# Kernel tuning notes

Hardware: AMD Instinct MI355X
Metric: run time of the kernel (lower is better)

The kernel has to match this reference:

```python
import jax, jax.numpy as jnp
import numpy as np

EPS = 1e-4


def bin_act(x):
    # row-wise standardize (torch std is unbiased, ddof=1) then XNOR-style binarize
    mu = x.mean(axis=1, keepdims=True)
    sd = x.std(axis=1, ddof=1, keepdims=True)
    xn = (x - mu) / (sd + EPS)
    alpha = jnp.abs(xn).mean(axis=1, keepdims=True)  # L1 norm / n
    return alpha * jnp.sign(xn)


def bin_linear(inp, w, b):
    # BinLinearFunction.forward: w_hat = sign(w) * (||w_row||_1 / n_in)
    n = w.shape[1]
    m = jnp.abs(w).sum(axis=1, keepdims=True) / n
    w_hat = jnp.sign(w) * m
    return inp @ w_hat.T + b


def scatter_mean(feat, dst, n_dst):
    s = jax.ops.segment_sum(feat, dst, num_segments=n_dst)
    cnt = jax.ops.segment_sum(jnp.ones(dst.shape, feat.dtype), dst, num_segments=n_dst)
    return s / jnp.maximum(cnt, 1.0)[:, None]


def sage_layer(x, src, dst, n_dst, w_rel, b_rel, w_root, b_root):
    xb = bin_act(x)
    xt = bin_act(x[:n_dst])
    agg = scatter_mean(xb[src], dst, n_dst)  # mean aggregation of binarized neighbors
    return bin_linear(agg, w_rel, b_rel) + bin_linear(xt, w_root, b_root)


def setup_inputs() -> dict:
    key = jax.random.key(0)
    ks = jax.random.split(key, 10)
    N0, N1, N2 = 512000, 20480, 2048
    E1, E2 = 512000, 20480
    IN, HID, OUT = 128, 256, 64
    x = jax.random.normal(ks[0], (N0, IN), dtype=jnp.float32)
    src1 = jax.random.randint(ks[1], (E1,), 0, N0)
    dst1 = jax.random.randint(ks[2], (E1,), 0, N1)
    src2 = jax.random.randint(ks[3], (E2,), 0, N1)
    dst2 = jax.random.randint(ks[4], (E2,), 0, N2)
    def winit(k, out_f, in_f):
        return jax.random.normal(k, (out_f, in_f), dtype=jnp.float32) * np.sqrt(1.0 / in_f)
    return {
        "x": x, "src1": src1, "dst1": dst1, "src2": src2, "dst2": dst2,
        "w_rel1": winit(ks[5], HID, IN), "b_rel1": jnp.zeros((HID,), jnp.float32),
        "w_root1": winit(ks[6], HID, IN), "b_root1": jnp.zeros((HID,), jnp.float32),
        "w_rel2": winit(ks[7], OUT, HID), "b_rel2": jnp.zeros((OUT,), jnp.float32),
        "w_root2": winit(ks[8], OUT, HID), "b_root2": jnp.zeros((OUT,), jnp.float32),
        "n1": N1, "n2": N2,
    }


def reference(x, src1, dst1, src2, dst2, w_rel1, b_rel1, w_root1, b_root1,
              w_rel2, b_rel2, w_root2, b_root2, n1, n2):
    h = sage_layer(x, src1, dst1, n1, w_rel1, b_rel1, w_root1, b_root1)
    h = jax.nn.relu(h)  # dropout p=0.0
    h = sage_layer(h, src2, dst2, n2, w_rel2, b_rel2, w_root2, b_root2)
    return jax.nn.log_softmax(h, axis=-1)
```

## Files before the change

kernel.cpp:

```cpp
#include <hip/hip_runtime.h>
#include <stdint.h>

typedef unsigned long long u64;


#define CAP1 128
#define CAP2 128

__device__ __forceinline__ void pack_row128(
    float4 v0, float4 v1, float4 v2, float4 v3, float mu, int c,
    u64& w0, u64& w1)
{
  unsigned m = 0;
  m |= (v0.x > mu) ? 1u << 0  : 0u;
  m |= (v0.y > mu) ? 1u << 1  : 0u;
  m |= (v0.z > mu) ? 1u << 2  : 0u;
  m |= (v0.w > mu) ? 1u << 3  : 0u;
  m |= (v1.x > mu) ? 1u << 4  : 0u;
  m |= (v1.y > mu) ? 1u << 5  : 0u;
  m |= (v1.z > mu) ? 1u << 6  : 0u;
  m |= (v1.w > mu) ? 1u << 7  : 0u;
  m |= (v2.x > mu) ? 1u << 8  : 0u;
  m |= (v2.y > mu) ? 1u << 9  : 0u;
  m |= (v2.z > mu) ? 1u << 10 : 0u;
  m |= (v2.w > mu) ? 1u << 11 : 0u;
  m |= (v3.x > mu) ? 1u << 12 : 0u;
  m |= (v3.y > mu) ? 1u << 13 : 0u;
  m |= (v3.z > mu) ? 1u << 14 : 0u;
  m |= (v3.w > mu) ? 1u << 15 : 0u;
  u64 wv = (u64)m << (16 * (c & 3));
  wv |= __shfl_xor(wv, 1);
  wv |= __shfl_xor(wv, 2);
  u64 other = __shfl_xor(wv, 4);
  w0 = (c & 4) ? other : wv;
  w1 = (c & 4) ? wv : other;
}

__device__ __forceinline__ void prep_w128_block(
    const float* __restrict__ w, int rowbase, int tid,
    ulonglong2* __restrict__ wbits, float* __restrict__ m)
{
  int lane = tid & 63;
  int g = lane >> 3, c = lane & 7;
  int row = rowbase + (tid >> 6) * 8 + g;
  const float4* wr = (const float4*)(w + (size_t)row * 128);
  float4 v0 = wr[c];
  float4 v1 = wr[c + 8];
  float4 v2 = wr[c + 16];
  float4 v3 = wr[c + 24];
  float s = fabsf(v0.x) + fabsf(v0.y) + fabsf(v0.z) + fabsf(v0.w)
          + fabsf(v1.x) + fabsf(v1.y) + fabsf(v1.z) + fabsf(v1.w)
          + fabsf(v2.x) + fabsf(v2.y) + fabsf(v2.z) + fabsf(v2.w)
          + fabsf(v3.x) + fabsf(v3.y) + fabsf(v3.z) + fabsf(v3.w);
  s += __shfl_xor(s, 1); s += __shfl_xor(s, 2); s += __shfl_xor(s, 4);
  u64 w0, w1;
  pack_row128(v0, v1, v2, v3, 0.0f, c, w0, w1);
  if (c == 0) {
    wbits[row] = make_ulonglong2(w0, w1);
    m[row] = s * (1.0f / 128.0f);
  }
}

__device__ __forceinline__ void prep_w256_block(
    const float* __restrict__ w, int rowbase, int tid,
    u64* __restrict__ wbits, float* __restrict__ m)
{
  int lane = tid & 63;
  int o = rowbase + (tid >> 6);
  const float* wr = w + (size_t)o * 256;
  float s = 0.0f;
  u64 b[4];
  #pragma unroll
  for (int wd = 0; wd < 4; wd++) {
    float v = wr[wd * 64 + lane];
    s += fabsf(v);
    b[wd] = __ballot(v > 0.0f);
  }
  #pragma unroll
  for (int off = 32; off > 0; off >>= 1) s += __shfl_xor(s, off);
  if (lane == 0) {
    wbits[o * 4 + 0] = b[0]; wbits[o * 4 + 1] = b[1];
    wbits[o * 4 + 2] = b[2]; wbits[o * 4 + 3] = b[3];
    m[o] = s * (1.0f / 256.0f);
  }
}

__global__ __launch_bounds__(256) void prep_all_kernel(
    const float* __restrict__ w_rel1, const float* __restrict__ w_root1,
    const float* __restrict__ w_rel2, const float* __restrict__ w_root2,
    ulonglong2* __restrict__ wbr1, float* __restrict__ m_r1,
    ulonglong2* __restrict__ wbt1, float* __restrict__ m_t1,
    u64* __restrict__ wbr2, float* __restrict__ m_r2,
    u64* __restrict__ wbt2, float* __restrict__ m_t2,
    int* __restrict__ cnt, int cntn)
{
  int b = blockIdx.x, t = threadIdx.x;
  if (b < 8) {
    prep_w128_block(w_rel1, b * 32, t, wbr1, m_r1);
  } else if (b < 16) {
    prep_w128_block(w_root1, (b - 8) * 32, t, wbt1, m_t1);
  } else if (b < 32) {
    prep_w256_block(w_rel2, (b - 16) * 4, t, wbr2, m_r2);
  } else if (b < 48) {
    prep_w256_block(w_root2, (b - 32) * 4, t, wbt2, m_t2);
  } else {
    int base = (b - 48) * 2048 + t * 8;
    #pragma unroll
    for (int k = 0; k < 8; k++) {
      int i = base + k;
      if (i < cntn) cnt[i] = 0;
    }
  }
}

__global__ void scatter_direct_kernel(
    const int* __restrict__ dst1, const int* __restrict__ src1, int E1,
    int* __restrict__ cnt1, int* __restrict__ slots1,
    const int* __restrict__ dst2, const int* __restrict__ src2, int E2,
    int* __restrict__ cnt2, int* __restrict__ slots2)
{
  int i = blockIdx.x * blockDim.x + threadIdx.x;
  if (i < E1) {
    int dd = dst1[i];
    int p = atomicAdd(&cnt1[dd], 1);
    if (p < CAP1) slots1[(size_t)dd * CAP1 + p] = src1[i];
  } else if (i < E1 + E2) {
    int j = i - E1;
    int dd = dst2[j];
    int p = atomicAdd(&cnt2[dd], 1);
    if (p < CAP2) slots2[(size_t)dd * CAP2 + p] = src2[j];
  }
}

__global__ __launch_bounds__(256) void binact128_kernel(
    const float* __restrict__ x, ulonglong2* __restrict__ bits1,
    float* __restrict__ alpha1)
{
  int lane = threadIdx.x & 63;
  int wid  = blockIdx.x * 4 + (threadIdx.x >> 6);
  int g = lane >> 3;
  int c = lane & 7;
  int row = wid * 8 + g;
  const float4* xr = (const float4*)(x + (size_t)row * 128);
  float4 v0 = xr[c];
  float4 v1 = xr[c + 8];
  float4 v2 = xr[c + 16];
  float4 v3 = xr[c + 24];

  float s = (v0.x + v0.y + v0.z + v0.w) + (v1.x + v1.y + v1.z + v1.w)
          + (v2.x + v2.y + v2.z + v2.w) + (v3.x + v3.y + v3.z + v3.w);
  s += __shfl_xor(s, 1); s += __shfl_xor(s, 2); s += __shfl_xor(s, 4);
  float mu = s * (1.0f / 128.0f);

  float ss = 0.f, sa = 0.f;
  {
    float d;
    d = v0.x - mu; ss += d * d; sa += fabsf(d);
    d = v0.y - mu; ss += d * d; sa += fabsf(d);
    d = v0.z - mu; ss += d * d; sa += fabsf(d);
    d = v0.w - mu; ss += d * d; sa += fabsf(d);
    d = v1.x - mu; ss += d * d; sa += fabsf(d);
    d = v1.y - mu; ss += d * d; sa += fabsf(d);
    d = v1.z - mu; ss += d * d; sa += fabsf(d);
    d = v1.w - mu; ss += d * d; sa += fabsf(d);
    d = v2.x - mu; ss += d * d; sa += fabsf(d);
    d = v2.y - mu; ss += d * d; sa += fabsf(d);
    d = v2.z - mu; ss += d * d; sa += fabsf(d);
    d = v2.w - mu; ss += d * d; sa += fabsf(d);
    d = v3.x - mu; ss += d * d; sa += fabsf(d);
    d = v3.y - mu; ss += d * d; sa += fabsf(d);
    d = v3.z - mu; ss += d * d; sa += fabsf(d);
    d = v3.w - mu; ss += d * d; sa += fabsf(d);
  }
  ss += __shfl_xor(ss, 1); ss += __shfl_xor(ss, 2); ss += __shfl_xor(ss, 4);
  sa += __shfl_xor(sa, 1); sa += __shfl_xor(sa, 2); sa += __shfl_xor(sa, 4);
  float sd = sqrtf(ss * (1.0f / 127.0f));
  float a  = __fdividef(sa * (1.0f / 128.0f), sd + 1e-4f);

  u64 w0, w1;
  pack_row128(v0, v1, v2, v3, mu, c, w0, w1);
  if (c == 0) {
    bits1[row] = make_ulonglong2(w0, w1);
    alpha1[row] = a;
  }
}

__global__ __launch_bounds__(256) void layer1_kernel(
    const ulonglong2* __restrict__ bits1, const float* __restrict__ alpha1,
    const int* __restrict__ cnt, const int* __restrict__ slots,
    const ulonglong2* __restrict__ wb_rel, const float* __restrict__ m_rel,
    const float* __restrict__ b_rel,
    const ulonglong2* __restrict__ wb_root, const float* __restrict__ m_root,
    const float* __restrict__ b_root,
    u64* __restrict__ bits2, float* __restrict__ alpha2)
{
  int lane = threadIdx.x & 63;
  int d = blockIdx.x * 4 + (threadIdx.x >> 6);

  ulonglong2 wr[4], wt[4];
  float mr[4], br[4], mt[4], bt[4];
  #pragma unroll
  for (int j = 0; j < 4; j++) {
    int f = j * 64 + lane;
    wr[j] = wb_rel[f];  mr[j] = m_rel[f];  br[j] = b_rel[f];
    wt[j] = wb_root[f]; mt[j] = m_root[f]; bt[j] = b_root[f];
  }

  int deg = cnt[d];
  int degc = min(deg, CAP1);
  const int* slot = slots + (size_t)d * CAP1;

  float acc2[4] = {0.f, 0.f, 0.f, 0.f};
  float suma = 0.f;

  #pragma unroll 4
  for (int e = 0; e < degc; e++) {
    int sn = __builtin_amdgcn_readfirstlane(slot[e]);
    ulonglong2 bb = bits1[sn];
    float a = alpha1[sn];
    suma += a;
    #pragma unroll
    for (int j = 0; j < 4; j++) {
      int pc = __popcll(bb.x ^ wr[j].x) + __popcll(bb.y ^ wr[j].y);
      acc2[j] += a * (float)pc;
    }
  }

  ulonglong2 xb = bits1[d];
  float ax = alpha1[d];

  float invc = (deg > 0) ? 1.0f / (float)deg : 1.0f;
  float z[4];
  #pragma unroll
  for (int j = 0; j < 4; j++) {
    int pcr = __popcll(xb.x ^ wt[j].x) + __popcll(xb.y ^ wt[j].y);
    float rel = mr[j] * (128.0f * suma - 2.0f * acc2[j]) * invc + br[j];
    float rot = mt[j] * ax * (float)(128 - 2 * pcr) + bt[j];
    z[j] = fmaxf(rel + rot, 0.0f);
  }

  float s = z[0] + z[1] + z[2] + z[3];
  #pragma unroll
  for (int off = 1; off < 64; off <<= 1) s += __shfl_xor(s, off);
  float mu = s * (1.0f / 256.0f);
  float ss = 0.f, sa = 0.f;
  #pragma unroll
  for (int j = 0; j < 4; j++) {
    float dv = z[j] - mu;
    ss += dv * dv; sa += fabsf(dv);
  }
  #pragma unroll
  for (int off = 1; off < 64; off <<= 1) {
    ss += __shfl_xor(ss, off);
    sa += __shfl_xor(sa, off);
  }
  float sd = sqrtf(ss * (1.0f / 255.0f));
  float a2 = __fdividef(sa * (1.0f / 256.0f), sd + 1e-4f);
  u64 wd0 = __ballot(z[0] > mu);
  u64 wd1 = __ballot(z[1] > mu);
  u64 wd2 = __ballot(z[2] > mu);
  u64 wd3 = __ballot(z[3] > mu);
  if (lane == 0) {
    ulonglong2* bp = (ulonglong2*)(bits2 + (size_t)d * 4);
    bp[0] = make_ulonglong2(wd0, wd1);
    bp[1] = make_ulonglong2(wd2, wd3);
    alpha2[d] = a2;
  }
}

__global__ __launch_bounds__(256) void layer2_kernel(
    const u64* __restrict__ bits2, const float* __restrict__ alpha2,
    const int* __restrict__ cnt, const int* __restrict__ slots,
    const u64* __restrict__ wb_rel, const float* __restrict__ m_rel,
    const float* __restrict__ b_rel,
    const u64* __restrict__ wb_root, const float* __restrict__ m_root,
    const float* __restrict__ b_root,
    float* __restrict__ out)
{
  int d = blockIdx.x * 4 + (threadIdx.x >> 6);
  int o = threadIdx.x & 63;
  u64 w0 = wb_rel[o * 4 + 0], w1 = wb_rel[o * 4 + 1];
  u64 w2 = wb_rel[o * 4 + 2], w3 = wb_rel[o * 4 + 3];
  int deg = cnt[d];
  int degc = min(deg, CAP2);
  const int* slot = slots + (size_t)d * CAP2;
  float acc = 0.0f;
  #pragma unroll 2
  for (int e = 0; e < degc; e++) {
    int sn = __builtin_amdgcn_readfirstlane(slot[e]);
    const ulonglong2* bp = (const ulonglong2*)(bits2 + (size_t)sn * 4);
    ulonglong2 p0 = bp[0], p1 = bp[1];
    float a = alpha2[sn];
    int pc = __popcll(p0.x ^ w0) + __popcll(p0.y ^ w1)
           + __popcll(p1.x ^ w2) + __popcll(p1.y ^ w3);
    acc += a * (float)(256 - 2 * pc);
  }
  float invc = 1.0f / (float)(deg > 0 ? deg : 1);
  const u64* xp = bits2 + (size_t)d * 4;
  float ax = alpha2[d];
  int pcr = __popcll(xp[0] ^ wb_root[o * 4 + 0]) + __popcll(xp[1] ^ wb_root[o * 4 + 1])
          + __popcll(xp[2] ^ wb_root[o * 4 + 2]) + __popcll(xp[3] ^ wb_root[o * 4 + 3]);
  float z = m_rel[o] * acc * invc + b_rel[o]
          + m_root[o] * ax * (float)(256 - 2 * pcr) + b_root[o];
  float mx = z;
  #pragma unroll
  for (int off = 32; off > 0; off >>= 1) mx = fmaxf(mx, __shfl_xor(mx, off));
  float ex = expf(z - mx);
  float se = ex;
  #pragma unroll
  for (int off = 32; off > 0; off >>= 1) se += __shfl_xor(se, off);
  out[(size_t)d * 64 + o] = z - mx - logf(se);
}

extern "C" void kernel_launch(void* const* d_in, const int* in_sizes, int n_in,
                              void* d_out, int out_size, void* d_ws, size_t ws_size,
                              hipStream_t stream)
{
  const float* x       = (const float*)d_in[0];
  const int*   src1    = (const int*)d_in[1];
  const int*   dst1    = (const int*)d_in[2];
  const int*   src2    = (const int*)d_in[3];
  const int*   dst2    = (const int*)d_in[4];
  const float* w_rel1  = (const float*)d_in[5];
  const float* b_rel1  = (const float*)d_in[6];
  const float* w_root1 = (const float*)d_in[7];
  const float* b_root1 = (const float*)d_in[8];
  const float* w_rel2  = (const float*)d_in[9];
  const float* b_rel2  = (const float*)d_in[10];
  const float* w_root2 = (const float*)d_in[11];
  const float* b_root2 = (const float*)d_in[12];

  const int IN  = 128;
  const int HID = in_sizes[6];
  const int OUT = in_sizes[10];
  const int N0  = in_sizes[0] / IN;
  const int E1  = in_sizes[1];
  const int E2  = in_sizes[3];
  const int N1  = 20480;
  const int N2  = out_size / OUT;
  (void)n_in; (void)ws_size;

  char* p = (char*)d_ws;
  auto alloc = [&](size_t bytes) {
    char* r = p;
    p += (bytes + 255) & ~(size_t)255;
    return r;
  };
  ulonglong2* bits1 = (ulonglong2*)alloc((size_t)N0 * 16);
  float* alpha1 = (float*)alloc((size_t)N0 * 4);
  u64*   bits2  = (u64*)alloc((size_t)N1 * 32);
  float* alpha2 = (float*)alloc((size_t)N1 * 4);
  int*   slots1 = (int*)alloc((size_t)N1 * CAP1 * 4);
  int*   slots2 = (int*)alloc((size_t)N2 * CAP2 * 4);
  int*   cnt1   = (int*)alloc((size_t)(N1 + N2) * 4);
  int*   cnt2   = cnt1 + N1;
  ulonglong2* wbr1 = (ulonglong2*)alloc((size_t)HID * 16);
  ulonglong2* wbt1 = (ulonglong2*)alloc((size_t)HID * 16);
  u64*   wbr2   = (u64*)alloc((size_t)OUT * 32);
  u64*   wbt2   = (u64*)alloc((size_t)OUT * 32);
  float* m_r1   = (float*)alloc((size_t)HID * 4);
  float* m_t1   = (float*)alloc((size_t)HID * 4);
  float* m_r2   = (float*)alloc((size_t)OUT * 4);
  float* m_t2   = (float*)alloc((size_t)OUT * 4);

  prep_all_kernel<<<59, 256, 0, stream>>>(
      w_rel1, w_root1, w_rel2, w_root2,
      wbr1, m_r1, wbt1, m_t1, wbr2, m_r2, wbt2, m_t2,
      cnt1, N1 + N2);

  scatter_direct_kernel<<<(E1 + E2 + 255) / 256, 256, 0, stream>>>(
      dst1, src1, E1, cnt1, slots1, dst2, src2, E2, cnt2, slots2);

  binact128_kernel<<<N0 / 32, 256, 0, stream>>>(x, bits1, alpha1);

  layer1_kernel<<<N1 / 4, 256, 0, stream>>>(bits1, alpha1, cnt1, slots1,
                                            wbr1, m_r1, b_rel1, wbt1, m_t1, b_root1,
                                            bits2, alpha2);

  layer2_kernel<<<N2 / 4, 256, 0, stream>>>(bits2, alpha2, cnt2, slots2,
                                            wbr2, m_r2, b_rel2, wbt2, m_t2, b_root2,
                                            (float*)d_out);
}
```

Measured before the change: 482.6 us.

## Skip binarizing unreferenced source rows and pack bits with alpha records

The scatter pass now marks every source node referenced by a layer-1 edge. The binarization kernel then skips unmarked rows beyond the first N1, which it still always processes. Bits and alpha are stored together in one 32-byte record so each neighbor gather fetches a single contiguous chunk, and x is read with nontemporal loads. This adds a byte-mark array, its zeroing, and extra scattered byte writes per edge.

```diff
diff --git a/kernel.cpp b/kernel.cpp
--- a/kernel.cpp
+++ b/kernel.cpp
@@ -2,6 +2,7 @@
 #include <stdint.h>
 
 typedef unsigned long long u64;
+typedef float nfloat4 __attribute__((ext_vector_type(4)));
 
 
 #define CAP1 128
@@ -92,7 +93,8 @@
     ulonglong2* __restrict__ wbt1, float* __restrict__ m_t1,
     u64* __restrict__ wbr2, float* __restrict__ m_r2,
     u64* __restrict__ wbt2, float* __restrict__ m_t2,
-    int* __restrict__ cnt, int cntn)
+    int* __restrict__ cnt, int cntn,
+    int* __restrict__ markw, int markn)
 {
   int b = blockIdx.x, t = threadIdx.x;
   if (b < 8) {
@@ -103,13 +105,20 @@
     prep_w256_block(w_rel2, (b - 16) * 4, t, wbr2, m_r2);
   } else if (b < 48) {
     prep_w256_block(w_root2, (b - 32) * 4, t, wbt2, m_t2);
-  } else {
+  } else if (b < 59) {
     int base = (b - 48) * 2048 + t * 8;
     #pragma unroll
     for (int k = 0; k < 8; k++) {
       int i = base + k;
       if (i < cntn) cnt[i] = 0;
     }
+  } else {
+    int base = (b - 59) * 2048 + t * 8;
+    #pragma unroll
+    for (int k = 0; k < 8; k++) {
+      int i = base + k;
+      if (i < markn) markw[i] = 0;
+    }
   }
 }
 
@@ -117,13 +126,16 @@
     const int* __restrict__ dst1, const int* __restrict__ src1, int E1,
     int* __restrict__ cnt1, int* __restrict__ slots1,
     const int* __restrict__ dst2, const int* __restrict__ src2, int E2,
-    int* __restrict__ cnt2, int* __restrict__ slots2)
+    int* __restrict__ cnt2, int* __restrict__ slots2,
+    unsigned char* __restrict__ mark)
 {
   int i = blockIdx.x * blockDim.x + threadIdx.x;
   if (i < E1) {
+    int s = src1[i];
+    mark[s] = 1;
     int dd = dst1[i];
     int p = atomicAdd(&cnt1[dd], 1);
-    if (p < CAP1) slots1[(size_t)dd * CAP1 + p] = src1[i];
+    if (p < CAP1) slots1[(size_t)dd * CAP1 + p] = s;
   } else if (i < E1 + E2) {
     int j = i - E1;
     int dd = dst2[j];
@@ -133,19 +145,25 @@
 }
 
 __global__ __launch_bounds__(256) void binact128_kernel(
-    const float* __restrict__ x, ulonglong2* __restrict__ bits1,
-    float* __restrict__ alpha1)
+    const float* __restrict__ x, const unsigned char* __restrict__ mark,
+    int n1, u64* __restrict__ rec)
 {
   int lane = threadIdx.x & 63;
   int wid  = blockIdx.x * 4 + (threadIdx.x >> 6);
   int g = lane >> 3;
   int c = lane & 7;
   int row = wid * 8 + g;
-  const float4* xr = (const float4*)(x + (size_t)row * 128);
-  float4 v0 = xr[c];
-  float4 v1 = xr[c + 8];
-  float4 v2 = xr[c + 16];
-  float4 v3 = xr[c + 24];
+  if (row >= n1 && mark[row] == 0) return;
+
+  const nfloat4* xr = (const nfloat4*)(x + (size_t)row * 128);
+  nfloat4 n0 = __builtin_nontemporal_load(xr + c);
+  nfloat4 n1v = __builtin_nontemporal_load(xr + c + 8);
+  nfloat4 n2 = __builtin_nontemporal_load(xr + c + 16);
+  nfloat4 n3 = __builtin_nontemporal_load(xr + c + 24);
+  float4 v0 = make_float4(n0.x, n0.y, n0.z, n0.w);
+  float4 v1 = make_float4(n1v.x, n1v.y, n1v.z, n1v.w);
+  float4 v2 = make_float4(n2.x, n2.y, n2.z, n2.w);
+  float4 v3 = make_float4(n3.x, n3.y, n3.z, n3.w);
 
   float s = (v0.x + v0.y + v0.z + v0.w) + (v1.x + v1.y + v1.z + v1.w)
           + (v2.x + v2.y + v2.z + v2.w) + (v3.x + v3.y + v3.z + v3.w);
@@ -180,13 +198,14 @@
   u64 w0, w1;
   pack_row128(v0, v1, v2, v3, mu, c, w0, w1);
   if (c == 0) {
-    bits1[row] = make_ulonglong2(w0, w1);
-    alpha1[row] = a;
+    u64* rp = rec + (size_t)row * 4;
+    *(ulonglong2*)rp = make_ulonglong2(w0, w1);
+    ((float*)rp)[4] = a;
   }
 }
 
 __global__ __launch_bounds__(256) void layer1_kernel(
-    const ulonglong2* __restrict__ bits1, const float* __restrict__ alpha1,
+    const u64* __restrict__ rec,
     const int* __restrict__ cnt, const int* __restrict__ slots,
     const ulonglong2* __restrict__ wb_rel, const float* __restrict__ m_rel,
     const float* __restrict__ b_rel,
@@ -216,8 +235,9 @@
   #pragma unroll 4
   for (int e = 0; e < degc; e++) {
     int sn = __builtin_amdgcn_readfirstlane(slot[e]);
-    ulonglong2 bb = bits1[sn];
-    float a = alpha1[sn];
+    const u64* rp = rec + (size_t)sn * 4;
+    ulonglong2 bb = *(const ulonglong2*)rp;
+    float a = ((const float*)rp)[4];
     suma += a;
     #pragma unroll
     for (int j = 0; j < 4; j++) {
@@ -226,8 +246,9 @@
     }
   }
 
-  ulonglong2 xb = bits1[d];
-  float ax = alpha1[d];
+  const u64* rd = rec + (size_t)d * 4;
+  ulonglong2 xb = *(const ulonglong2*)rd;
+  float ax = ((const float*)rd)[4];
 
   float invc = (deg > 0) ? 1.0f / (float)deg : 1.0f;
   float z[4];
@@ -346,14 +367,14 @@
     p += (bytes + 255) & ~(size_t)255;
     return r;
   };
-  ulonglong2* bits1 = (ulonglong2*)alloc((size_t)N0 * 16);
-  float* alpha1 = (float*)alloc((size_t)N0 * 4);
+  u64*   rec    = (u64*)alloc((size_t)N0 * 32);
   u64*   bits2  = (u64*)alloc((size_t)N1 * 32);
   float* alpha2 = (float*)alloc((size_t)N1 * 4);
   int*   slots1 = (int*)alloc((size_t)N1 * CAP1 * 4);
   int*   slots2 = (int*)alloc((size_t)N2 * CAP2 * 4);
   int*   cnt1   = (int*)alloc((size_t)(N1 + N2) * 4);
   int*   cnt2   = cnt1 + N1;
+  unsigned char* mark = (unsigned char*)alloc((size_t)N0);
   ulonglong2* wbr1 = (ulonglong2*)alloc((size_t)HID * 16);
   ulonglong2* wbt1 = (ulonglong2*)alloc((size_t)HID * 16);
   u64*   wbr2   = (u64*)alloc((size_t)OUT * 32);
@@ -363,17 +384,17 @@
   float* m_r2   = (float*)alloc((size_t)OUT * 4);
   float* m_t2   = (float*)alloc((size_t)OUT * 4);
 
-  prep_all_kernel<<<59, 256, 0, stream>>>(
+  prep_all_kernel<<<122, 256, 0, stream>>>(
       w_rel1, w_root1, w_rel2, w_root2,
       wbr1, m_r1, wbt1, m_t1, wbr2, m_r2, wbt2, m_t2,
-      cnt1, N1 + N2);
+      cnt1, N1 + N2, (int*)mark, N0 / 4);
 
   scatter_direct_kernel<<<(E1 + E2 + 255) / 256, 256, 0, stream>>>(
-      dst1, src1, E1, cnt1, slots1, dst2, src2, E2, cnt2, slots2);
-
-  binact128_kernel<<<N0 / 32, 256, 0, stream>>>(x, bits1, alpha1);
-
-  layer1_kernel<<<N1 / 4, 256, 0, stream>>>(bits1, alpha1, cnt1, slots1,
+      dst1, src1, E1, cnt1, slots1, dst2, src2, E2, cnt2, slots2, mark);
+
+  binact128_kernel<<<N0 / 32, 256, 0, stream>>>(x, mark, N1, rec);
+
+  layer1_kernel<<<N1 / 4, 256, 0, stream>>>(rec, cnt1, slots1,
                                             wbr1, m_r1, b_rel1, wbt1, m_t1, b_root1,
                                             bits2, alpha2);
 
```

Measured after the change: 458.7 us. 5.0% less time.
